# Kernel optimization log

Hardware: AMD Instinct MI355X
Metric: run time of the kernel (lower is better)

The kernel has to match this reference:

```python
import jax, jax.numpy as jnp
import numpy as np

B, S, D = 2, 1024, 1024
NH = 8
QK = 512   # qk_dim = 0.5 * D
V = 1024   # v_dim = 1.0 * D
DQK = QK // NH   # 64
DHV = V // NH    # 128
CAP = 15.0       # gate_soft_cap
NORM_EPS = 1e-6
DENOM_EPS = 1e-6


def soft_cap(x, cap):
    return cap * jnp.tanh(x / cap)


def setup_inputs() -> dict:
    key = jax.random.key(0)
    ks = jax.random.split(key, 8)
    s = 0.02
    return {
        "x": jax.random.normal(ks[0], (B, S, D), jnp.float32),
        "Wq": jax.random.normal(ks[1], (QK, D), jnp.float32) * s,
        "Wk": jax.random.normal(ks[2], (QK, D), jnp.float32) * s,
        "Wv": jax.random.normal(ks[3], (V, D), jnp.float32) * s,
        "Wog": jax.random.normal(ks[4], (V, D), jnp.float32) * s,
        "Wi": jax.random.normal(ks[5], (NH, D), jnp.float32) * s,
        "bi": jnp.zeros((NH,), jnp.float32),
        "Wf": jax.random.normal(ks[6], (NH, D), jnp.float32) * s,
        "bf": jnp.ones((NH,), jnp.float32),  # positive forget bias
        "gamma": jnp.ones((V,), jnp.float32),
        "Wout": jax.random.normal(ks[7], (D, V), jnp.float32) * s,
    }


def _mlstm_recurrent(q, k, v, i_pre, f_pre):
    # q,k: [B,S,NH,DQK]; v: [B,S,NH,DHV]; i_pre,f_pre: [B,S,NH]
    f_log = jax.nn.log_sigmoid(f_pre)
    q_s = q * (DQK ** -0.5)
    # move time to leading axis for scan
    xs = (jnp.moveaxis(q_s, 1, 0), jnp.moveaxis(k, 1, 0), jnp.moveaxis(v, 1, 0),
          jnp.moveaxis(i_pre, 1, 0), jnp.moveaxis(f_log, 1, 0))
    C0 = jnp.zeros((B, NH, DQK, DHV), q.dtype)
    n0 = jnp.zeros((B, NH, DQK), q.dtype)
    m0 = jnp.zeros((B, NH), q.dtype)

    def step(carry, xt):
        C, n, m = carry
        qt, kt, vt, it, ft = xt  # [B,NH,*]
        m_new = jnp.maximum(ft + m, it)                      # [B,NH]
        f_act = jnp.exp(ft + m - m_new)
        i_act = jnp.exp(it - m_new)
        C = f_act[..., None, None] * C + i_act[..., None, None] * (kt[..., :, None] * vt[..., None, :])
        n = f_act[..., None] * n + i_act[..., None] * kt
        h_num = jnp.einsum('bhd,bhdv->bhv', qt, C)
        qn = jnp.einsum('bhd,bhd->bh', qt, n)
        denom = jnp.maximum(jnp.abs(qn), jnp.exp(-m_new)) + DENOM_EPS
        h = h_num / denom[..., None]
        return (C, n, m_new), h

    (C, n, m), hs = jax.lax.scan(step, (C0, n0, m0), xs)
    return jnp.moveaxis(hs, 0, 1), (C, n, m)  # h: [B,S,NH,DHV]


def reference(x, Wq, Wk, Wv, Wog, Wi, bi, Wf, bf, gamma, Wout):
    q = (x @ Wq.T).reshape(B, S, NH, DQK)
    k = (x @ Wk.T).reshape(B, S, NH, DQK)
    v = (x @ Wv.T).reshape(B, S, NH, DHV)
    o_pre = x @ Wog.T                                  # [B,S,V]
    i_pre = soft_cap(x @ Wi.T + bi, CAP)               # [B,S,NH]
    f_pre = soft_cap(x @ Wf.T + bf, CAP)               # [B,S,NH]

    h, _state = _mlstm_recurrent(q, k, v, i_pre, f_pre)  # [B,S,NH,DHV]

    # multi-head layernorm over head dim, float32 reductions
    h32 = h.astype(jnp.float32)
    mu = jnp.mean(h32, axis=-1, keepdims=True)
    var = jnp.mean(jnp.square(h32 - mu), axis=-1, keepdims=True)
    h_norm = ((h32 - mu) * jax.lax.rsqrt(var + NORM_EPS)).astype(h.dtype)
    h_norm = h_norm * gamma.reshape(NH, DHV)
    h_norm = h_norm.reshape(B, S, V)

    h_out = jax.nn.sigmoid(o_pre) * h_norm
    y = h_out @ Wout.T
    return y
```

## Files before the change

kernel.cpp:

```cpp
#include <hip/hip_runtime.h>
#include <hip/hip_bf16.h>
#include <math.h>

typedef __bf16 bf16x8 __attribute__((ext_vector_type(8)));
typedef float f32x4 __attribute__((ext_vector_type(4)));

#define NB 2
#define NS 1024
#define ND 1024
#define NH 8
#define NQK 512
#define NV 1024
#define DQK 64
#define DHV 128
#define CHUNK 64
#define NCHUNK 16

#define GLDS16(g, l) __builtin_amdgcn_global_load_lds((const __attribute__((address_space(1))) void*)(g), (__attribute__((address_space(3))) void*)(l), 16, 0, 0)

static __device__ __forceinline__ void split_bf16(float v, __bf16& hi, __bf16& lo) {
  hi = (__bf16)v;
  lo = (__bf16)(v - (float)hi);
}

static __device__ __forceinline__ int xcd_swz(int orig, int nwg) {
  int q = nwg >> 3, r = nwg & 7;
  int xcd = orig & 7, idx = orig >> 3;
  int base = (xcd < r) ? xcd * (q + 1) : r * (q + 1) + (xcd - r) * q;
  return base + idx;
}

__global__ __launch_bounds__(256) void prep_kernel(const float* __restrict__ x,
    const float* __restrict__ wq, const float* __restrict__ wk,
    const float* __restrict__ wv, const float* __restrict__ wog,
    const float* __restrict__ wout,
    const float* __restrict__ Wi, const float* __restrict__ bi,
    const float* __restrict__ Wf, const float* __restrict__ bf_,
    __bf16* __restrict__ xb, __bf16* __restrict__ wb, __bf16* __restrict__ wob,
    float* __restrict__ icap, float* __restrict__ flog) {
  if (blockIdx.x < 6144) {
    long i = (long)blockIdx.x * 256 + threadIdx.x;
    const float* src; __bf16* dst;
    if (i < 524288)        { src = x    + i*4;                    dst = xb  + i*4; }
    else if (i < 655360)   { long j = i -  524288; src = wq  + j*4; dst = wb + j*4; }
    else if (i < 786432)   { long j = i -  655360; src = wk  + j*4; dst = wb +  524288 + j*4; }
    else if (i < 1048576)  { long j = i -  786432; src = wv  + j*4; dst = wb + 1048576 + j*4; }
    else if (i < 1310720)  { long j = i - 1048576; src = wog + j*4; dst = wb + 2097152 + j*4; }
    else                   { long j = i - 1310720; src = wout+ j*4; dst = wob + j*4; }
    float4 v = *(const float4*)src;
    __bf16 o[4];
    o[0] = (__bf16)v.x; o[1] = (__bf16)v.y; o[2] = (__bf16)v.z; o[3] = (__bf16)v.w;
    *(short4*)dst = *(const short4*)o;
  } else {
    const int row = blockIdx.x - 6144;
    const int w = threadIdx.x >> 6;
    const int l = threadIdx.x & 63;
    const float* xr = x + (size_t)row * ND;
    float xv[16];
    #pragma unroll
    for (int t = 0; t < 16; ++t) xv[t] = xr[l + 64*t];
    for (int hh = 0; hh < 2; ++hh) {
      int h = w*2 + hh;
      const float* wi = Wi + (size_t)h * ND;
      const float* wf = Wf + (size_t)h * ND;
      float si = 0.f, sf = 0.f;
      #pragma unroll
      for (int t = 0; t < 16; ++t) {
        si += xv[t] * wi[l + 64*t];
        sf += xv[t] * wf[l + 64*t];
      }
      #pragma unroll
      for (int off = 32; off; off >>= 1) {
        si += __shfl_xor(si, off, 64);
        sf += __shfl_xor(sf, off, 64);
      }
      if (l == 0) {
        float ic = 15.f * tanhf((si + bi[h]) * (1.f/15.f));
        float fc = 15.f * tanhf((sf + bf_[h]) * (1.f/15.f));
        float fl = (fc >= 0.f) ? -log1pf(__expf(-fc)) : (fc - log1pf(__expf(fc)));
        icap[row*NH + h] = ic;
        flog[row*NH + h] = fl;
      }
    }
  }
}

#define STAGE_AB(Abuf, Bbuf, Aptr, Bptr, Krun, ktv)                           \
  do {                                                                        \
    _Pragma("unroll")                                                         \
    for (int i_ = 0; i_ < 4; ++i_) {                                          \
      const int sb_ = i_ * 256 + wid * 64;                                    \
      const int s_ = sb_ + lane;                                              \
      const int row_ = s_ >> 3;                                               \
      const int klog_ = (s_ & 7) ^ (row_ & 7);                                \
      GLDS16(Aptr + (size_t)(m0 + row_) * Krun + (ktv) * 64 + klog_ * 8, Abuf + sb_ * 8); \
      if (i_ < 2)                                                             \
        GLDS16(Bptr + (size_t)(n0 + row_) * Krun + (ktv) * 64 + klog_ * 8, Bbuf + sb_ * 8); \
    }                                                                         \
  } while (0)

__global__ __launch_bounds__(256) void gemm_bt(const __bf16* __restrict__ A,
                                               const __bf16* __restrict__ Bm,
                                               float* __restrict__ C,
                                               int M, int N, int K, int ntn, int nwg) {
  __shared__ __bf16 smA[2][128 * 64];
  __shared__ __bf16 smB[2][64 * 64];
  const int wg = xcd_swz(blockIdx.x, nwg);
  const int m0 = (wg / ntn) * 128;
  const int n0 = (wg % ntn) * 64;
  const int tid = threadIdx.x;
  const int wid = tid >> 6, lane = tid & 63;
  const int wm = (wid >> 1) * 64, wn = (wid & 1) * 32;
  const int fr = lane & 15;
  const int g  = lane >> 4;
  f32x4 acc[4][2] = {};
  const int NT = K >> 6;
  STAGE_AB(smA[0], smB[0], A, Bm, K, 0);
  int cur = 0;
  for (int kt = 0; kt < NT; ++kt) {
    __syncthreads();
    if (kt + 1 < NT) STAGE_AB(smA[cur ^ 1], smB[cur ^ 1], A, Bm, K, kt + 1);
    #pragma unroll
    for (int kk = 0; kk < 2; ++kk) {
      const int kg = kk * 4 + g;
      bf16x8 af[4], bfv[2];
      #pragma unroll
      for (int f = 0; f < 4; ++f) {
        const int Ra = wm + f * 16 + fr;
        af[f] = *(const bf16x8*)&smA[cur][Ra * 64 + ((kg ^ (Ra & 7)) * 8)];
      }
      #pragma unroll
      for (int n = 0; n < 2; ++n) {
        const int Rb = wn + n * 16 + fr;
        bfv[n] = *(const bf16x8*)&smB[cur][Rb * 64 + ((kg ^ (Rb & 7)) * 8)];
      }
      #pragma unroll
      for (int i = 0; i < 4; ++i)
        #pragma unroll
        for (int j = 0; j < 2; ++j)
          acc[i][j] = __builtin_amdgcn_mfma_f32_16x16x32_bf16(af[i], bfv[j], acc[i][j], 0, 0, 0);
    }
    cur ^= 1;
  }
  const int orow = m0 + wm + g * 4;
  const int ocol = n0 + wn + fr;
  #pragma unroll
  for (int i = 0; i < 4; ++i)
    #pragma unroll
    for (int j = 0; j < 2; ++j)
      #pragma unroll
      for (int r = 0; r < 4; ++r)
        C[(size_t)(orow + i*16 + r) * N + (ocol + j*16)] = acc[i][j][r];
}

__global__ __launch_bounds__(256) void gemm_proj(const __bf16* __restrict__ A,
    const __bf16* __restrict__ Bm,
    __bf16* __restrict__ qh, __bf16* __restrict__ ql,
    __bf16* __restrict__ kh, __bf16* __restrict__ kl,
    __bf16* __restrict__ kT, __bf16* __restrict__ vT,
    _Float16* __restrict__ ogs) {
  __shared__ __bf16 smA[2][128 * 64];
  __shared__ __bf16 smB[2][64 * 64];
  const int wg = xcd_swz(blockIdx.x, 768);
  const int m0 = (wg / 48) * 128;
  const int n0 = (wg % 48) * 64;
  const int tid = threadIdx.x;
  const int wid = tid >> 6, lane = tid & 63;
  const int wm = (wid >> 1) * 64, wn = (wid & 1) * 32;
  const int fr = lane & 15;
  const int g  = lane >> 4;
  f32x4 acc[4][2] = {};
  STAGE_AB(smA[0], smB[0], A, Bm, 1024, 0);
  int cur = 0;
  for (int kt = 0; kt < 16; ++kt) {
    __syncthreads();
    if (kt + 1 < 16) STAGE_AB(smA[cur ^ 1], smB[cur ^ 1], A, Bm, 1024, kt + 1);
    #pragma unroll
    for (int kk = 0; kk < 2; ++kk) {
      const int kg = kk * 4 + g;
      bf16x8 af[4], bfv[2];
      #pragma unroll
      for (int f = 0; f < 4; ++f) {
        const int Ra = wm + f * 16 + fr;
        af[f] = *(const bf16x8*)&smA[cur][Ra * 64 + ((kg ^ (Ra & 7)) * 8)];
      }
      #pragma unroll
      for (int n = 0; n < 2; ++n) {
        const int Rb = wn + n * 16 + fr;
        bfv[n] = *(const bf16x8*)&smB[cur][Rb * 64 + ((kg ^ (Rb & 7)) * 8)];
      }
      #pragma unroll
      for (int i = 0; i < 4; ++i)
        #pragma unroll
        for (int j = 0; j < 2; ++j)
          acc[i][j] = __builtin_amdgcn_mfma_f32_16x16x32_bf16(af[i], bfv[j], acc[i][j], 0, 0, 0);
    }
    cur ^= 1;
  }
  const int orow = m0 + wm + g * 4;
  const int ocol = n0 + wn + fr;
  const int rng = n0 >> 9;
  if (rng == 0 || rng == 1) {
    __bf16* Hb = (rng == 0) ? qh : kh;
    __bf16* Lb = (rng == 0) ? ql : kl;
    const float sc = (rng == 0) ? 0.125f : 1.0f;
    #pragma unroll
    for (int i = 0; i < 4; ++i)
      #pragma unroll
      for (int j = 0; j < 2; ++j) {
        const int col = (ocol + j*16) & 511;
        const int d = col & 63;
        const int hb = col & ~63;
        __bf16 t4[4];
        #pragma unroll
        for (int r = 0; r < 4; ++r) {
          const int row = orow + i*16 + r;
          float v = acc[i][j][r] * sc;
          __bf16 hi, lo; split_bf16(v, hi, lo);
          t4[r] = hi;
          const int off = row*512 + hb + ((((d>>3) ^ (row&7))) << 3) + (d & 7);
          Hb[off] = hi;
          Lb[off] = lo;
        }
        if (rng == 1) {
          const int row0r = orow + i*16;
          const int bh = ((row0r >> 10) << 3) + (col >> 6);
          const int c = (row0r >> 6) & 15;
          const int s0 = (row0r & 63);
          const int off = ((bh*16 + c)*64 + d)*64 + (((s0>>3) ^ (d&7)) << 3) + (s0 & 7);
          *(short4*)&kT[off] = *(const short4*)t4;
        }
      }
  } else if (rng == 2 || rng == 3) {
    #pragma unroll
    for (int i = 0; i < 4; ++i)
      #pragma unroll
      for (int j = 0; j < 2; ++j) {
        const int col = (ocol + j*16) & 1023;
        const int u = col & 127;
        __bf16 t4[4];
        #pragma unroll
        for (int r = 0; r < 4; ++r) t4[r] = (__bf16)acc[i][j][r];
        const int row0r = orow + i*16;
        const int bh = ((row0r >> 10) << 3) + (col >> 7);
        const int c = (row0r >> 6) & 15;
        const int s0 = (row0r & 63);
        const int off = ((bh*16 + c)*128 + u)*64 + (((s0>>3) ^ (u&7)) << 3) + (s0 & 7);
        *(short4*)&vT[off] = *(const short4*)t4;
      }
  } else {
    #pragma unroll
    for (int i = 0; i < 4; ++i)
      #pragma unroll
      for (int j = 0; j < 2; ++j) {
        const int col = (ocol + j*16) & 1023;
        #pragma unroll
        for (int r = 0; r < 4; ++r) {
          const int row = orow + i*16 + r;
          float sg = 1.f / (1.f + __expf(-acc[i][j][r]));
          ogs[(size_t)row*1024 + col] = (_Float16)sg;
        }
      }
  }
}

__global__ __launch_bounds__(64) void gates_kernel(const float* __restrict__ icap,
    const float* __restrict__ flog, float* __restrict__ g_g, float* __restrict__ a_g,
    float* __restrict__ m_g, float* __restrict__ m0g) {
  const int bh = blockIdx.x;
  const int b = bh >> 3, h = bh & 7;
  const int l = threadIdx.x;
  float m0 = 0.f;
  for (int c = 0; c < NCHUNK; ++c) {
    const int t = c*CHUNK + l;
    const int row = b*NS + t;
    float B = flog[row*NH + h];
    float iv = icap[row*NH + h];
    #pragma unroll
    for (int d = 1; d < 64; d <<= 1) {
      float o = __shfl_up(B, d, 64);
      if (l >= d) B += o;
    }
    float g = iv - B;
    float cm = g;
    #pragma unroll
    for (int d = 1; d < 64; d <<= 1) {
      float o = __shfl_up(cm, d, 64);
      if (l >= d) cm = fmaxf(cm, o);
    }
    float a = fmaxf(m0, cm);
    float m = B + a;
    const int idx = bh*NS + t;
    g_g[idx] = g; a_g[idx] = a; m_g[idx] = m;
    if (l == 0) m0g[bh*NCHUNK + c] = m0;
    m0 = __shfl(m, 63, 64);
  }
}

__global__ __launch_bounds__(256) void u_kernel(const __bf16* __restrict__ kT,
    const __bf16* __restrict__ vT, const float* __restrict__ g_g,
    const float* __restrict__ a_g, float* __restrict__ Ut, float* __restrict__ Ung) {
  __shared__ float w_l[64];
  const int task = blockIdx.x;
  const int bh = task >> 4, c = task & 15;
  const int t = threadIdx.x;
  const int wid = t >> 6, lane = t & 63;
  const int fr = lane & 15, g = lane >> 4;
  if (t < 64) {
    const float aL = a_g[bh*NS + c*CHUNK + 63];
    w_l[t] = __expf(g_g[bh*NS + c*CHUNK + t] - aL);
  }
  __syncthreads();
  const __bf16* ktb = kT + (size_t)task * 4096;
  const __bf16* vtb = vT + (size_t)task * 8192;
  f32x4 acc[8] = {};
  #pragma unroll
  for (int kk = 0; kk < 2; ++kk) {
    const int kg = kk*4 + g;
    const int Ra = wid*16 + fr;
    bf16x8 afr = *(const bf16x8*)&ktb[Ra*64 + ((kg ^ (Ra & 7)) * 8)];
    bf16x8 afw;
    #pragma unroll
    for (int j = 0; j < 8; ++j) afw[j] = (__bf16)((float)afr[j] * w_l[kg*8 + j]);
    #pragma unroll
    for (int nt = 0; nt < 8; ++nt) {
      const int Rb = nt*16 + fr;
      bf16x8 bv = *(const bf16x8*)&vtb[Rb*64 + ((kg ^ (Rb & 7)) * 8)];
      acc[nt] = __builtin_amdgcn_mfma_f32_16x16x32_bf16(afw, bv, acc[nt], 0, 0, 0);
    }
  }
  float* ub = Ut + (size_t)task * 8192;
  #pragma unroll
  for (int nt = 0; nt < 8; ++nt) {
    const int u = nt*16 + fr;
    *(f32x4*)&ub[u*64 + wid*16 + g*4] = acc[nt];
  }
  if (t < 64) {
    float s = 0.f;
    #pragma unroll
    for (int blk = 0; blk < 8; ++blk) {
      bf16x8 kv = *(const bf16x8*)&ktb[t*64 + ((blk ^ (t & 7)) * 8)];
      #pragma unroll
      for (int j = 0; j < 8; ++j) s += (float)kv[j] * w_l[blk*8 + j];
    }
    Ung[task*64 + t] = s;
  }
}

__global__ __launch_bounds__(64) void statescan_kernel(const float* __restrict__ Ut,
    const float* __restrict__ Ung, const float* __restrict__ m0g,
    const float* __restrict__ a_g, __bf16* __restrict__ C0T, float* __restrict__ n0g) {
  const int bh = blockIdx.x >> 4, part = blockIdx.x & 15;
  const int e8 = part*64 + threadIdx.x;
  const int u = e8 >> 3, d8 = e8 & 7;
  const int dsto = u*64 + ((d8 ^ (u & 7)) << 3);
  const int srco = u*64 + d8*8;
  float scale[NCHUNK];
  #pragma unroll
  for (int c = 0; c < NCHUNK; ++c)
    scale[c] = __expf(m0g[bh*NCHUNK + c] - a_g[bh*NS + c*CHUNK + 63]);
  float val[8] = {};
  for (int c = 0; c < NCHUNK; ++c) {
    const size_t base = ((size_t)(bh*NCHUNK + c)) * 8192;
    __bf16 o[8];
    #pragma unroll
    for (int j = 0; j < 8; ++j) o[j] = (__bf16)val[j];
    *(float4*)&C0T[base + dsto] = *(const float4*)o;
    f32x4 u0 = *(const f32x4*)&Ut[base + srco];
    f32x4 u1 = *(const f32x4*)&Ut[base + srco + 4];
    #pragma unroll
    for (int j = 0; j < 4; ++j) {
      val[j]   = scale[c]*val[j]   + u0[j];
      val[j+4] = scale[c]*val[j+4] + u1[j];
    }
  }
  if (part == 0) {
    float nv = 0.f;
    for (int c = 0; c < NCHUNK; ++c) {
      int idx = (bh*NCHUNK + c)*64 + threadIdx.x;
      n0g[idx] = nv;
      nv = scale[c]*nv + Ung[idx];
    }
  }
}

__global__ __launch_bounds__(256) void intra_kernel(
    const __bf16* __restrict__ qh, const __bf16* __restrict__ ql,
    const __bf16* __restrict__ kh, const __bf16* __restrict__ kl,
    const __bf16* __restrict__ vT, const __bf16* __restrict__ C0T,
    const _Float16* __restrict__ ogs,
    const float* __restrict__ g_g, const float* __restrict__ a_g,
    const float* __restrict__ m_g, const float* __restrict__ m0g,
    const float* __restrict__ n0g,
    const float* __restrict__ gamma, __bf16* __restrict__ hout) {
  __shared__ __bf16 Ps[32*72];
  __shared__ float g_l[64], n0_l[64], a_l[32], m_l[32], cI_l[32];
  __shared__ float qnA[2][32], qnI_l[32], lnS[2][32], lnQ[2][32];

  const int blk = blockIdx.x;
  const int task = blk >> 1, jhalf = blk & 1;
  const int bh = task >> 4, c = task & 15;
  const int b = bh >> 3, h = bh & 7;
  const int t = threadIdx.x;
  const int wid = t >> 6, lane = t & 63;
  const int fr = lane & 15, lg = lane >> 4;
  const int jt_local = wid >> 1, half = wid & 1;
  const int jtg = jhalf*2 + jt_local;
  const int row0 = b*NS + c*CHUNK;
  const int jrow0 = row0 + jhalf*32;
  const __bf16* vtb = vT + (size_t)task * 8192;
  const __bf16* c0b = C0T + (size_t)task * 8192;

  const float m0v = m0g[bh*NCHUNK + c];
  if (t < 64) {
    g_l[t]  = g_g[bh*NS + c*CHUNK + t];
    n0_l[t] = n0g[task*64 + t];
  } else if (t < 96) {
    int jl = t - 64;
    float av = a_g[bh*NS + c*CHUNK + jhalf*32 + jl];
    a_l[jl] = av;
    m_l[jl] = m_g[bh*NS + c*CHUNK + jhalf*32 + jl];
    cI_l[jl] = __expf(m0v - av);
  }
  __syncthreads();

  const int Ra = jt_local*16 + fr;
  const size_t qrow = (size_t)(jrow0 + Ra)*512 + h*64;
  bf16x8 qhv[2], qlv[2];
  #pragma unroll
  for (int kk = 0; kk < 2; ++kk) {
    const int kg = kk*4 + lg;
    const int off = (kg ^ (Ra & 7)) * 8;
    qhv[kk] = *(const bf16x8*)&qh[qrow + off];
    qlv[kk] = *(const bf16x8*)&ql[qrow + off];
  }

  float rsum[4] = {0.f, 0.f, 0.f, 0.f};
  for (int st = half; st < 4; st += 2) {
    if (st <= jtg) {
      f32x4 sacc = {};
      const int Rb = st*16 + fr;
      const size_t krow = (size_t)(row0 + Rb)*512 + h*64;
      #pragma unroll
      for (int kk = 0; kk < 2; ++kk) {
        const int kg = kk*4 + lg;
        const int offb = (kg ^ (Rb & 7)) * 8;
        bf16x8 khv = *(const bf16x8*)&kh[krow + offb];
        bf16x8 klv = *(const bf16x8*)&kl[krow + offb];
        sacc = __builtin_amdgcn_mfma_f32_16x16x32_bf16(qhv[kk], khv, sacc, 0, 0, 0);
        sacc = __builtin_amdgcn_mfma_f32_16x16x32_bf16(qhv[kk], klv, sacc, 0, 0, 0);
        sacc = __builtin_amdgcn_mfma_f32_16x16x32_bf16(qlv[kk], khv, sacc, 0, 0, 0);
      }
      const int s_c = st*16 + fr;
      const float gs = g_l[s_c];
      #pragma unroll
      for (int r = 0; r < 4; ++r) {
        const int jl = jt_local*16 + lg*4 + r;
        const int j_c = jhalf*32 + jl;
        float w = (s_c <= j_c) ? __expf(gs - a_l[jl]) : 0.f;
        float p = sacc[r] * w;
        rsum[r] += p;
        Ps[jl*72 + s_c] = (__bf16)p;
      }
    } else {
      #pragma unroll
      for (int r = 0; r < 4; ++r)
        Ps[(jt_local*16 + lg*4 + r)*72 + st*16 + fr] = (__bf16)0.f;
    }
  }
  #pragma unroll
  for (int r = 0; r < 4; ++r) {
    #pragma unroll
    for (int off = 1; off < 16; off <<= 1) rsum[r] += __shfl_xor(rsum[r], off, 64);
  }
  if (fr == 0) {
    #pragma unroll
    for (int r = 0; r < 4; ++r) qnA[half][jt_local*16 + lg*4 + r] = rsum[r];
  }

  f32x4 acc[4] = {};
  #pragma unroll
  for (int kk = 0; kk < 2; ++kk) {
    const int kg = kk*4 + lg;
    #pragma unroll
    for (int nt = 0; nt < 4; ++nt) {
      const int Rb = (half*4 + nt)*16 + fr;
      bf16x8 bc = *(const bf16x8*)&c0b[Rb*64 + ((kg ^ (Rb&7))*8)];
      acc[nt] = __builtin_amdgcn_mfma_f32_16x16x32_bf16(qhv[kk], bc, acc[nt], 0, 0, 0);
    }
  }
  {
    float ci4[4];
    #pragma unroll
    for (int r = 0; r < 4; ++r) ci4[r] = cI_l[jt_local*16 + lg*4 + r];
    #pragma unroll
    for (int nt = 0; nt < 4; ++nt)
      #pragma unroll
      for (int r = 0; r < 4; ++r) acc[nt][r] *= ci4[r];
  }
  if (half == 1) {
    const int jl = jt_local*16 + fr;
    const size_t qr2 = (size_t)(jrow0 + jl)*512 + h*64;
    float s = 0.f;
    #pragma unroll
    for (int i = 0; i < 16; ++i) {
      const int d = lg*16 + i;
      const int off = (((d>>3) ^ (jl&7)) << 3) + (d & 7);
      float qv = (float)qh[qr2 + off] + (float)ql[qr2 + off];
      s += qv * n0_l[d];
    }
    s += __shfl_xor(s, 16, 64);
    s += __shfl_xor(s, 32, 64);
    if (lane < 16) qnI_l[jl] = cI_l[jl] * s;
  }
  __syncthreads();

  #pragma unroll
  for (int kk = 0; kk < 2; ++kk) {
    const int kg = kk*4 + lg;
    bf16x8 ap = *(const bf16x8*)&Ps[(jt_local*16 + fr)*72 + kg*8];
    #pragma unroll
    for (int nt = 0; nt < 4; ++nt) {
      const int Rb = (half*4 + nt)*16 + fr;
      bf16x8 bv = *(const bf16x8*)&vtb[Rb*64 + ((kg ^ (Rb&7))*8)];
      acc[nt] = __builtin_amdgcn_mfma_f32_16x16x32_bf16(ap, bv, acc[nt], 0, 0, 0);
    }
  }

  #pragma unroll
  for (int r = 0; r < 4; ++r) {
    const int jl = jt_local*16 + lg*4 + r;
    float qn = qnA[0][jl] + qnA[1][jl] + qnI_l[jl];
    float denom = fmaxf(fabsf(qn), __expf(-m_l[jl])) + 1e-6f;
    float rd = 1.f / denom;
    float s = 0.f, q2 = 0.f;
    #pragma unroll
    for (int nt = 0; nt < 4; ++nt) {
      float hv = acc[nt][r] * rd;
      acc[nt][r] = hv;
      s += hv; q2 += hv*hv;
    }
    #pragma unroll
    for (int off = 1; off < 16; off <<= 1) {
      s  += __shfl_xor(s,  off, 64);
      q2 += __shfl_xor(q2, off, 64);
    }
    if (fr == 0) { lnS[half][jl] = s; lnQ[half][jl] = q2; }
  }
  __syncthreads();

  #pragma unroll
  for (int r = 0; r < 4; ++r) {
    const int jl = jt_local*16 + lg*4 + r;
    float sm = lnS[0][jl] + lnS[1][jl];
    float sq = lnQ[0][jl] + lnQ[1][jl];
    float mu = sm * (1.f/128.f);
    float var = sq * (1.f/128.f) - mu*mu;
    float rstd = rsqrtf(var + 1e-6f);
    const int rowg = jrow0 + jl;
    #pragma unroll
    for (int nt = 0; nt < 4; ++nt) {
      const int u = (half*4 + nt)*16 + fr;
      float sg = (float)ogs[(size_t)rowg*1024 + h*DHV + u];
      float hn = (acc[nt][r] - mu) * rstd * gamma[h*DHV + u] * sg;
      hout[(size_t)rowg*NV + h*DHV + u] = (__bf16)hn;
    }
  }
}

extern "C" void kernel_launch(void* const* d_in, const int* in_sizes, int n_in,
                              void* d_out, int out_size, void* d_ws, size_t ws_size,
                              hipStream_t stream) {
  const float* x    = (const float*)d_in[0];
  const float* Wq   = (const float*)d_in[1];
  const float* Wk   = (const float*)d_in[2];
  const float* Wv   = (const float*)d_in[3];
  const float* Wog  = (const float*)d_in[4];
  const float* Wi   = (const float*)d_in[5];
  const float* bi   = (const float*)d_in[6];
  const float* Wf   = (const float*)d_in[7];
  const float* bf_  = (const float*)d_in[8];
  const float* gamma= (const float*)d_in[9];
  const float* Wout = (const float*)d_in[10];
  float* y = (float*)d_out;

  char* ws = (char*)d_ws;
  const size_t MB = 1u << 20;
  __bf16*   xb   = (__bf16*)  (ws + 0);
  __bf16*   Wb   = (__bf16*)  (ws + 4*MB);
  __bf16*   Wob  = (__bf16*)  (ws + 10*MB);
  __bf16*   qh   = (__bf16*)  (ws + 12*MB);
  __bf16*   ql   = (__bf16*)  (ws + 14*MB);
  __bf16*   kh   = (__bf16*)  (ws + 16*MB);
  __bf16*   kl   = (__bf16*)  (ws + 18*MB);
  __bf16*   kT   = (__bf16*)  (ws + 20*MB);
  __bf16*   vT   = (__bf16*)  (ws + 22*MB);
  _Float16* ogs  = (_Float16*)(ws + 26*MB);
  float*    Ut   = (float*)   (ws + 30*MB);
  __bf16*   C0T  = (__bf16*)  (ws + 38*MB);
  float*    icap = (float*)   (ws + 42*MB);
  float*    flog = (float*)   (ws + 42*MB + 64*1024);
  float*    g_g  = (float*)   (ws + 42*MB + 128*1024);
  float*    a_g  = (float*)   (ws + 42*MB + 192*1024);
  float*    m_g  = (float*)   (ws + 42*MB + 256*1024);
  float*    m0g  = (float*)   (ws + 42*MB + 320*1024);
  float*    Ung  = (float*)   (ws + 42*MB + 384*1024);
  float*    n0g  = (float*)   (ws + 42*MB + 448*1024);
  __bf16*   houtb= (__bf16*)  (ws + 44*MB);

  prep_kernel<<<8192, 256, 0, stream>>>(x, Wq, Wk, Wv, Wog, Wout, Wi, bi, Wf, bf_,
                                        xb, Wb, Wob, icap, flog);

  gemm_proj<<<768, 256, 0, stream>>>(xb, Wb, qh, ql, kh, kl, kT, vT, ogs);

  gates_kernel<<<16, 64, 0, stream>>>(icap, flog, g_g, a_g, m_g, m0g);
  u_kernel<<<256, 256, 0, stream>>>(kT, vT, g_g, a_g, Ut, Ung);
  statescan_kernel<<<256, 64, 0, stream>>>(Ut, Ung, m0g, a_g, C0T, n0g);
  intra_kernel<<<512, 256, 0, stream>>>(qh, ql, kh, kl, vT, C0T, ogs,
                                        g_g, a_g, m_g, m0g, n0g, gamma, houtb);

  gemm_bt<<<256, 256, 0, stream>>>(houtb, Wob, y, 2048, 1024, 1024, 16, 256);
}
```

Baseline: 163.4 us.

## Shrink output GEMM tile to 64x64 and merge intra-chunk blocks into 1024-thread block

The final output GEMM moves from 128x64 to 64x64 tiles, doubling the grid to 512 workgroups so the 256 compute units get more than one wave of work. The intra-chunk kernel now handles a whole 64-row chunk per 1024-thread block (16 waves, each doing one 16x16 score tile and a quarter of the value columns) instead of splitting it across two 256-thread blocks. That removes the duplicated loads of the chunk's state and value tiles and the idle masked score tiles. The cost is less data reuse per GEMM tile and a large block whose occupancy and barriers may limit overlap.

Measured after the change: 161.9 us. Within noise of the previous version (-0.9%).

```diff
diff --git a/kernel.cpp b/kernel.cpp
--- a/kernel.cpp
+++ b/kernel.cpp
@@ -99,33 +99,46 @@
     }                                                                         \
   } while (0)
 
+#define STAGE64(Abuf, Bbuf, Aptr, Bptr, Krun, ktv)                            \
+  do {                                                                        \
+    _Pragma("unroll")                                                         \
+    for (int i_ = 0; i_ < 2; ++i_) {                                          \
+      const int sb_ = i_ * 256 + wid * 64;                                    \
+      const int s_ = sb_ + lane;                                              \
+      const int row_ = s_ >> 3;                                               \
+      const int klog_ = (s_ & 7) ^ (row_ & 7);                                \
+      GLDS16(Aptr + (size_t)(m0 + row_) * Krun + (ktv) * 64 + klog_ * 8, Abuf + sb_ * 8); \
+      GLDS16(Bptr + (size_t)(n0 + row_) * Krun + (ktv) * 64 + klog_ * 8, Bbuf + sb_ * 8); \
+    }                                                                         \
+  } while (0)
+
 __global__ __launch_bounds__(256) void gemm_bt(const __bf16* __restrict__ A,
                                                const __bf16* __restrict__ Bm,
                                                float* __restrict__ C,
                                                int M, int N, int K, int ntn, int nwg) {
-  __shared__ __bf16 smA[2][128 * 64];
+  __shared__ __bf16 smA[2][64 * 64];
   __shared__ __bf16 smB[2][64 * 64];
   const int wg = xcd_swz(blockIdx.x, nwg);
-  const int m0 = (wg / ntn) * 128;
+  const int m0 = (wg / ntn) * 64;
   const int n0 = (wg % ntn) * 64;
   const int tid = threadIdx.x;
   const int wid = tid >> 6, lane = tid & 63;
-  const int wm = (wid >> 1) * 64, wn = (wid & 1) * 32;
+  const int wm = (wid >> 1) * 32, wn = (wid & 1) * 32;
   const int fr = lane & 15;
   const int g  = lane >> 4;
-  f32x4 acc[4][2] = {};
+  f32x4 acc[2][2] = {};
   const int NT = K >> 6;
-  STAGE_AB(smA[0], smB[0], A, Bm, K, 0);
+  STAGE64(smA[0], smB[0], A, Bm, K, 0);
   int cur = 0;
   for (int kt = 0; kt < NT; ++kt) {
     __syncthreads();
-    if (kt + 1 < NT) STAGE_AB(smA[cur ^ 1], smB[cur ^ 1], A, Bm, K, kt + 1);
+    if (kt + 1 < NT) STAGE64(smA[cur ^ 1], smB[cur ^ 1], A, Bm, K, kt + 1);
     #pragma unroll
     for (int kk = 0; kk < 2; ++kk) {
       const int kg = kk * 4 + g;
-      bf16x8 af[4], bfv[2];
-      #pragma unroll
-      for (int f = 0; f < 4; ++f) {
+      bf16x8 af[2], bfv[2];
+      #pragma unroll
+      for (int f = 0; f < 2; ++f) {
         const int Ra = wm + f * 16 + fr;
         af[f] = *(const bf16x8*)&smA[cur][Ra * 64 + ((kg ^ (Ra & 7)) * 8)];
       }
@@ -135,7 +148,7 @@
         bfv[n] = *(const bf16x8*)&smB[cur][Rb * 64 + ((kg ^ (Rb & 7)) * 8)];
       }
       #pragma unroll
-      for (int i = 0; i < 4; ++i)
+      for (int i = 0; i < 2; ++i)
         #pragma unroll
         for (int j = 0; j < 2; ++j)
           acc[i][j] = __builtin_amdgcn_mfma_f32_16x16x32_bf16(af[i], bfv[j], acc[i][j], 0, 0, 0);
@@ -145,7 +158,7 @@
   const int orow = m0 + wm + g * 4;
   const int ocol = n0 + wn + fr;
   #pragma unroll
-  for (int i = 0; i < 4; ++i)
+  for (int i = 0; i < 2; ++i)
     #pragma unroll
     for (int j = 0; j < 2; ++j)
       #pragma unroll
@@ -384,7 +397,7 @@
   }
 }
 
-__global__ __launch_bounds__(256) void intra_kernel(
+__global__ __launch_bounds__(1024) void intra_kernel(
     const __bf16* __restrict__ qh, const __bf16* __restrict__ ql,
     const __bf16* __restrict__ kh, const __bf16* __restrict__ kl,
     const __bf16* __restrict__ vT, const __bf16* __restrict__ C0T,
@@ -393,21 +406,18 @@
     const float* __restrict__ m_g, const float* __restrict__ m0g,
     const float* __restrict__ n0g,
     const float* __restrict__ gamma, __bf16* __restrict__ hout) {
-  __shared__ __bf16 Ps[32*72];
-  __shared__ float g_l[64], n0_l[64], a_l[32], m_l[32], cI_l[32];
-  __shared__ float qnA[2][32], qnI_l[32], lnS[2][32], lnQ[2][32];
-
-  const int blk = blockIdx.x;
-  const int task = blk >> 1, jhalf = blk & 1;
+  __shared__ __bf16 Ps[64*72];
+  __shared__ float g_l[64], n0_l[64], a_l[64], m_l[64], cI_l[64];
+  __shared__ float qnA_p[4][64], qnI_l[64], lnS_p[4][64], lnQ_p[4][64];
+
+  const int task = blockIdx.x;
   const int bh = task >> 4, c = task & 15;
   const int b = bh >> 3, h = bh & 7;
   const int t = threadIdx.x;
-  const int wid = t >> 6, lane = t & 63;
+  const int w = t >> 6, lane = t & 63;
   const int fr = lane & 15, lg = lane >> 4;
-  const int jt_local = wid >> 1, half = wid & 1;
-  const int jtg = jhalf*2 + jt_local;
+  const int jt = w >> 2, sl = w & 3;
   const int row0 = b*NS + c*CHUNK;
-  const int jrow0 = row0 + jhalf*32;
   const __bf16* vtb = vT + (size_t)task * 8192;
   const __bf16* c0b = C0T + (size_t)task * 8192;
 
@@ -415,17 +425,17 @@
   if (t < 64) {
     g_l[t]  = g_g[bh*NS + c*CHUNK + t];
     n0_l[t] = n0g[task*64 + t];
-  } else if (t < 96) {
+  } else if (t < 128) {
     int jl = t - 64;
-    float av = a_g[bh*NS + c*CHUNK + jhalf*32 + jl];
+    float av = a_g[bh*NS + c*CHUNK + jl];
     a_l[jl] = av;
-    m_l[jl] = m_g[bh*NS + c*CHUNK + jhalf*32 + jl];
+    m_l[jl] = m_g[bh*NS + c*CHUNK + jl];
     cI_l[jl] = __expf(m0v - av);
   }
   __syncthreads();
 
-  const int Ra = jt_local*16 + fr;
-  const size_t qrow = (size_t)(jrow0 + Ra)*512 + h*64;
+  const int Ra = jt*16 + fr;
+  const size_t qrow = (size_t)(row0 + Ra)*512 + h*64;
   bf16x8 qhv[2], qlv[2];
   #pragma unroll
   for (int kk = 0; kk < 2; ++kk) {
@@ -436,37 +446,34 @@
   }
 
   float rsum[4] = {0.f, 0.f, 0.f, 0.f};
-  for (int st = half; st < 4; st += 2) {
-    if (st <= jtg) {
-      f32x4 sacc = {};
-      const int Rb = st*16 + fr;
-      const size_t krow = (size_t)(row0 + Rb)*512 + h*64;
-      #pragma unroll
-      for (int kk = 0; kk < 2; ++kk) {
-        const int kg = kk*4 + lg;
-        const int offb = (kg ^ (Rb & 7)) * 8;
-        bf16x8 khv = *(const bf16x8*)&kh[krow + offb];
-        bf16x8 klv = *(const bf16x8*)&kl[krow + offb];
-        sacc = __builtin_amdgcn_mfma_f32_16x16x32_bf16(qhv[kk], khv, sacc, 0, 0, 0);
-        sacc = __builtin_amdgcn_mfma_f32_16x16x32_bf16(qhv[kk], klv, sacc, 0, 0, 0);
-        sacc = __builtin_amdgcn_mfma_f32_16x16x32_bf16(qlv[kk], khv, sacc, 0, 0, 0);
-      }
-      const int s_c = st*16 + fr;
-      const float gs = g_l[s_c];
-      #pragma unroll
-      for (int r = 0; r < 4; ++r) {
-        const int jl = jt_local*16 + lg*4 + r;
-        const int j_c = jhalf*32 + jl;
-        float w = (s_c <= j_c) ? __expf(gs - a_l[jl]) : 0.f;
-        float p = sacc[r] * w;
-        rsum[r] += p;
-        Ps[jl*72 + s_c] = (__bf16)p;
-      }
-    } else {
-      #pragma unroll
-      for (int r = 0; r < 4; ++r)
-        Ps[(jt_local*16 + lg*4 + r)*72 + st*16 + fr] = (__bf16)0.f;
-    }
+  if (sl <= jt) {
+    f32x4 sacc = {};
+    const int Rb = sl*16 + fr;
+    const size_t krow = (size_t)(row0 + Rb)*512 + h*64;
+    #pragma unroll
+    for (int kk = 0; kk < 2; ++kk) {
+      const int kg = kk*4 + lg;
+      const int offb = (kg ^ (Rb & 7)) * 8;
+      bf16x8 khv = *(const bf16x8*)&kh[krow + offb];
+      bf16x8 klv = *(const bf16x8*)&kl[krow + offb];
+      sacc = __builtin_amdgcn_mfma_f32_16x16x32_bf16(qhv[kk], khv, sacc, 0, 0, 0);
+      sacc = __builtin_amdgcn_mfma_f32_16x16x32_bf16(qhv[kk], klv, sacc, 0, 0, 0);
+      sacc = __builtin_amdgcn_mfma_f32_16x16x32_bf16(qlv[kk], khv, sacc, 0, 0, 0);
+    }
+    const int s_c = sl*16 + fr;
+    const float gs = g_l[s_c];
+    #pragma unroll
+    for (int r = 0; r < 4; ++r) {
+      const int jl = jt*16 + lg*4 + r;
+      float wgt = (s_c <= jl) ? __expf(gs - a_l[jl]) : 0.f;
+      float p = sacc[r] * wgt;
+      rsum[r] += p;
+      Ps[jl*72 + s_c] = (__bf16)p;
+    }
+  } else {
+    #pragma unroll
+    for (int r = 0; r < 4; ++r)
+      Ps[(jt*16 + lg*4 + r)*72 + sl*16 + fr] = (__bf16)0.f;
   }
   #pragma unroll
   for (int r = 0; r < 4; ++r) {
@@ -475,16 +482,16 @@
   }
   if (fr == 0) {
     #pragma unroll
-    for (int r = 0; r < 4; ++r) qnA[half][jt_local*16 + lg*4 + r] = rsum[r];
-  }
-
-  f32x4 acc[4] = {};
+    for (int r = 0; r < 4; ++r) qnA_p[sl][jt*16 + lg*4 + r] = rsum[r];
+  }
+
+  f32x4 acc[2] = {};
   #pragma unroll
   for (int kk = 0; kk < 2; ++kk) {
     const int kg = kk*4 + lg;
     #pragma unroll
-    for (int nt = 0; nt < 4; ++nt) {
-      const int Rb = (half*4 + nt)*16 + fr;
+    for (int nt = 0; nt < 2; ++nt) {
+      const int Rb = (sl*2 + nt)*16 + fr;
       bf16x8 bc = *(const bf16x8*)&c0b[Rb*64 + ((kg ^ (Rb&7))*8)];
       acc[nt] = __builtin_amdgcn_mfma_f32_16x16x32_bf16(qhv[kk], bc, acc[nt], 0, 0, 0);
     }
@@ -492,15 +499,15 @@
   {
     float ci4[4];
     #pragma unroll
-    for (int r = 0; r < 4; ++r) ci4[r] = cI_l[jt_local*16 + lg*4 + r];
-    #pragma unroll
-    for (int nt = 0; nt < 4; ++nt)
+    for (int r = 0; r < 4; ++r) ci4[r] = cI_l[jt*16 + lg*4 + r];
+    #pragma unroll
+    for (int nt = 0; nt < 2; ++nt)
       #pragma unroll
       for (int r = 0; r < 4; ++r) acc[nt][r] *= ci4[r];
   }
-  if (half == 1) {
-    const int jl = jt_local*16 + fr;
-    const size_t qr2 = (size_t)(jrow0 + jl)*512 + h*64;
+  if (sl == 3) {
+    const int jl = jt*16 + fr;
+    const size_t qr2 = (size_t)(row0 + jl)*512 + h*64;
     float s = 0.f;
     #pragma unroll
     for (int i = 0; i < 16; ++i) {
@@ -518,10 +525,10 @@
   #pragma unroll
   for (int kk = 0; kk < 2; ++kk) {
     const int kg = kk*4 + lg;
-    bf16x8 ap = *(const bf16x8*)&Ps[(jt_local*16 + fr)*72 + kg*8];
-    #pragma unroll
-    for (int nt = 0; nt < 4; ++nt) {
-      const int Rb = (half*4 + nt)*16 + fr;
+    bf16x8 ap = *(const bf16x8*)&Ps[(jt*16 + fr)*72 + kg*8];
+    #pragma unroll
+    for (int nt = 0; nt < 2; ++nt) {
+      const int Rb = (sl*2 + nt)*16 + fr;
       bf16x8 bv = *(const bf16x8*)&vtb[Rb*64 + ((kg ^ (Rb&7))*8)];
       acc[nt] = __builtin_amdgcn_mfma_f32_16x16x32_bf16(ap, bv, acc[nt], 0, 0, 0);
     }
@@ -529,13 +536,13 @@
 
   #pragma unroll
   for (int r = 0; r < 4; ++r) {
-    const int jl = jt_local*16 + lg*4 + r;
-    float qn = qnA[0][jl] + qnA[1][jl] + qnI_l[jl];
+    const int jl = jt*16 + lg*4 + r;
+    float qn = qnA_p[0][jl] + qnA_p[1][jl] + qnA_p[2][jl] + qnA_p[3][jl] + qnI_l[jl];
     float denom = fmaxf(fabsf(qn), __expf(-m_l[jl])) + 1e-6f;
     float rd = 1.f / denom;
     float s = 0.f, q2 = 0.f;
     #pragma unroll
-    for (int nt = 0; nt < 4; ++nt) {
+    for (int nt = 0; nt < 2; ++nt) {
       float hv = acc[nt][r] * rd;
       acc[nt][r] = hv;
       s += hv; q2 += hv*hv;
@@ -545,22 +552,22 @@
       s  += __shfl_xor(s,  off, 64);
       q2 += __shfl_xor(q2, off, 64);
     }
-    if (fr == 0) { lnS[half][jl] = s; lnQ[half][jl] = q2; }
+    if (fr == 0) { lnS_p[sl][jl] = s; lnQ_p[sl][jl] = q2; }
   }
   __syncthreads();
 
   #pragma unroll
   for (int r = 0; r < 4; ++r) {
-    const int jl = jt_local*16 + lg*4 + r;
-    float sm = lnS[0][jl] + lnS[1][jl];
-    float sq = lnQ[0][jl] + lnQ[1][jl];
+    const int jl = jt*16 + lg*4 + r;
+    float sm = lnS_p[0][jl] + lnS_p[1][jl] + lnS_p[2][jl] + lnS_p[3][jl];
+    float sq = lnQ_p[0][jl] + lnQ_p[1][jl] + lnQ_p[2][jl] + lnQ_p[3][jl];
     float mu = sm * (1.f/128.f);
     float var = sq * (1.f/128.f) - mu*mu;
     float rstd = rsqrtf(var + 1e-6f);
-    const int rowg = jrow0 + jl;
-    #pragma unroll
-    for (int nt = 0; nt < 4; ++nt) {
-      const int u = (half*4 + nt)*16 + fr;
+    const int rowg = row0 + jl;
+    #pragma unroll
+    for (int nt = 0; nt < 2; ++nt) {
+      const int u = (sl*2 + nt)*16 + fr;
       float sg = (float)ogs[(size_t)rowg*1024 + h*DHV + u];
       float hn = (acc[nt][r] - mu) * rstd * gamma[h*DHV + u] * sg;
       hout[(size_t)rowg*NV + h*DHV + u] = (__bf16)hn;
@@ -616,8 +623,8 @@
   gates_kernel<<<16, 64, 0, stream>>>(icap, flog, g_g, a_g, m_g, m0g);
   u_kernel<<<256, 256, 0, stream>>>(kT, vT, g_g, a_g, Ut, Ung);
   statescan_kernel<<<256, 64, 0, stream>>>(Ut, Ung, m0g, a_g, C0T, n0g);
-  intra_kernel<<<512, 256, 0, stream>>>(qh, ql, kh, kl, vT, C0T, ogs,
-                                        g_g, a_g, m_g, m0g, n0g, gamma, houtb);
-
-  gemm_bt<<<256, 256, 0, stream>>>(houtb, Wob, y, 2048, 1024, 1024, 16, 256);
-}
+  intra_kernel<<<256, 1024, 0, stream>>>(qh, ql, kh, kl, vT, C0T, ogs,
+                                         g_g, a_g, m_g, m0g, n0g, gamma, houtb);
+
+  gemm_bt<<<512, 256, 0, stream>>>(houtb, Wob, y, 2048, 1024, 1024, 16, 512);
+}
```
